# Optimization experiments

Measured on AMD Instinct MI355X. Metric: run time of the kernel, lower is better.

## Reference

```python
import jax, jax.numpy as jnp
import numpy as np

H = 512   # hidden_state_sizes
E = 512   # embedding_size
L = 2     # num_rnn_layers
VGG = 4096


def gru_cell(x, h, Wu, bu, Wr, br, Wc, bc):
    # stacked = cat(x, h) along features; rows of W: first input, then hidden
    s = jnp.concatenate([x, h], axis=1)
    r = jax.nn.sigmoid(s @ Wr + br)
    u = jax.nn.sigmoid(s @ Wu + bu)
    s1 = jnp.concatenate([x, r * h], axis=1)
    c = jnp.tanh(s1 @ Wc + bc)
    return u * h + (1.0 - u) * c


def setup_inputs() -> dict:
    key = jax.random.key(0)
    ks = jax.random.split(key, 10)
    B, T, V = 128, 40, 10000
    N = E + H  # concat width (layer0: E+H == H+H since E==H)
    sc = float(np.sqrt(1.0 / N))
    return dict(
        xTokens=jax.random.randint(ks[0], (B, T), 0, V),
        vgg_fc7=jax.random.normal(ks[1], (B, VGG), jnp.float32),
        embedding=jax.random.normal(ks[2], (V, E), jnp.float32) * 0.02,
        W_in=jax.random.normal(ks[3], (VGG, H), jnp.float32) * float(np.sqrt(1.0 / VGG)),
        b_in=jnp.zeros((H,), jnp.float32),
        W_u=jax.random.normal(ks[4], (L, N, H), jnp.float32) * sc,
        b_u=jnp.zeros((L, H), jnp.float32),
        W_r=jax.random.normal(ks[5], (L, N, H), jnp.float32) * sc,
        b_r=jnp.zeros((L, H), jnp.float32),
        W_c=jax.random.normal(ks[6], (L, N, H), jnp.float32) * sc,
        b_c=jnp.zeros((L, H), jnp.float32),
        W_out=jax.random.normal(ks[7], (H, V), jnp.float32) * float(np.sqrt(1.0 / H)),
        b_out=jnp.zeros((V,), jnp.float32),
    )


def reference(xTokens, vgg_fc7, embedding, W_in, b_in, W_u, b_u, W_r, b_r,
              W_c, b_c, W_out, b_out):
    # initial hidden state from image features, shared across rnn layers
    h0 = jnp.tanh(vgg_fc7 @ W_in + b_in)                # [B,H]
    h = jnp.broadcast_to(h0, (L,) + h0.shape)           # [L,B,H]
    x = embedding[xTokens]                              # [B,T,E]
    xs = jnp.swapaxes(x, 0, 1)                          # [T,B,E] (scan over time)

    def step(h, xt):
        hs = []
        inp = xt
        for j in range(L):  # small fixed layer loop
            hj = gru_cell(inp, h[j], W_u[j], b_u[j], W_r[j], b_r[j], W_c[j], b_c[j])
            hs.append(hj)
            inp = hj
        logit = inp @ W_out + b_out                     # [B,V]
        return jnp.stack(hs), logit

    h_final, logits = jax.lax.scan(step, h, xs)         # logits [T,B,V]
    return jnp.swapaxes(logits, 0, 1), h_final
```

## Files before the change

kernel.cpp:

```cpp
#include <hip/hip_runtime.h>
#include <hip/hip_bf16.h>
#include <math.h>

typedef __bf16 bf16_t;
typedef __bf16 bf16x8 __attribute__((ext_vector_type(8)));
typedef float  f32x4 __attribute__((ext_vector_type(4)));
typedef float  f4    __attribute__((ext_vector_type(4)));
typedef float  f2    __attribute__((ext_vector_type(2)));
typedef unsigned short u16x4 __attribute__((ext_vector_type(4)));
typedef unsigned long long u64;

#define HS  512
#define BB  128
#define TT  40
#define VV  10000
#define VGGN 4096
#define SLOT ((size_t)65536)
#define NBLK 96
#define NGRID 256

#define CL(h, idx) ((((h) * 164) + (idx)) * 64)
#define CRH0(h,s) CL(h, (s))
#define CHB0(h,s) CL(h, 41 + (s))
#define CRH1(h,s) CL(h, 82 + (s))
#define CHB1(h,s) CL(h, 123 + (s))
#define NSYNCW (328 * 64)

__device__ __forceinline__ void cst64(void* p, u64 v) {
  __hip_atomic_store((u64*)p, v, __ATOMIC_RELAXED, __HIP_MEMORY_SCOPE_AGENT);
}

__device__ __forceinline__ void slot_inc(unsigned* sync, int line)
{
  __syncthreads();
  asm volatile("" ::: "memory");
  if (threadIdx.x == 0)
    __hip_atomic_fetch_add(&sync[line], 1u, __ATOMIC_RELAXED,
                           __HIP_MEMORY_SCOPE_AGENT);
}

template<int SLP>
__device__ __forceinline__ void slot_wait(unsigned* sync, int line,
                                          unsigned target)
{
  if (threadIdx.x == 0) {
    while (__hip_atomic_load(&sync[line], __ATOMIC_RELAXED,
                             __HIP_MEMORY_SCOPE_AGENT) < target)
      __builtin_amdgcn_s_sleep(SLP);
  }
  asm volatile("" ::: "memory");
  __syncthreads();
}

template<int SLP>
__device__ __forceinline__ void slot_wait2(unsigned* sync, int lineA,
                                           unsigned tA, int lineB, unsigned tB)
{
  if (threadIdx.x == 0) {
    while (__hip_atomic_load(&sync[lineA], __ATOMIC_RELAXED,
                             __HIP_MEMORY_SCOPE_AGENT) < tA)
      __builtin_amdgcn_s_sleep(SLP);
    while (__hip_atomic_load(&sync[lineB], __ATOMIC_RELAXED,
                             __HIP_MEMORY_SCOPE_AGENT) < tB)
      __builtin_amdgcn_s_sleep(SLP);
  }
  asm volatile("" ::: "memory");
  __syncthreads();
}

__global__ void zero_sync(unsigned* p)
{
  for (int i = threadIdx.x; i < NSYNCW; i += 256) p[i] = 0u;
}

__global__ __launch_bounds__(256) void gemm_bt(
    const bf16_t* __restrict__ A, const bf16_t* __restrict__ Bt,
    const float* __restrict__ bias, float* __restrict__ C,
    int Nvalid, int ldc, int permute_tb)
{
  const int bm = blockIdx.x * 128, bn = blockIdx.y * 128;
  const int tid = threadIdx.x;
  const int wave = tid >> 6, lane = tid & 63;
  const int wm = (wave >> 1) * 64, wn = (wave & 1) * 64;
  const int l15 = lane & 15, kg = lane >> 4;
  const bf16_t* Ap = A + (size_t)(bm + wm + l15) * 512 + kg * 8;
  const bf16_t* Bp = Bt + (size_t)(bn + wn + l15) * 512 + kg * 8;
  f32x4 acc[4][4];
#pragma unroll
  for (int i = 0; i < 4; ++i)
#pragma unroll
    for (int j = 0; j < 4; ++j)
#pragma unroll
      for (int e = 0; e < 4; ++e) acc[i][j][e] = 0.f;

  for (int kk = 0; kk < 512; kk += 32) {
    bf16x8 a[4], b[4];
#pragma unroll
    for (int i = 0; i < 4; ++i) a[i] = *(const bf16x8*)(Ap + (size_t)i * 16 * 512 + kk);
#pragma unroll
    for (int j = 0; j < 4; ++j) b[j] = *(const bf16x8*)(Bp + (size_t)j * 16 * 512 + kk);
#pragma unroll
    for (int i = 0; i < 4; ++i)
#pragma unroll
      for (int j = 0; j < 4; ++j)
        acc[i][j] = __builtin_amdgcn_mfma_f32_16x16x32_bf16(a[i], b[j], acc[i][j], 0, 0, 0);
  }

#pragma unroll
  for (int fm = 0; fm < 4; ++fm) {
#pragma unroll
    for (int fn = 0; fn < 4; ++fn) {
      int n = bn + wn + fn * 16 + l15;
      if (n >= Nvalid) continue;
      float bv = bias ? bias[n] : 0.f;
#pragma unroll
      for (int e = 0; e < 4; ++e) {
        int m = bm + wm + fm * 16 + kg * 4 + e;
        int orow = permute_tb ? ((m & 127) * TT + (m >> 7)) : m;
        C[(size_t)orow * ldc + n] = acc[fm][fn][e] + bv;
      }
    }
  }
}

struct PArgs {
  const bf16_t *Btru0, *Bt1ru, *Btc0, *Btc1;
  const float  *xg0, *bu, *br, *bc, *hs0init;
  bf16_t *hb0_seq, *hb1_seq, *rh0s, *rh1s;
  const bf16_t *Wto;
  const float  *bo;
  float *out, *out_hfin;
  unsigned *sync;
};

template<int K, int NF>
__device__ __forceinline__ void tile_gemm64(
    const bf16_t* __restrict__ A0, const bf16_t* __restrict__ A1,
    const bf16_t* Bs, int wave, int lane, f32x4 (&acc)[NF])
{
  const int l15 = lane & 15, kg = lane >> 4;
  const int mw = wave * 16;
#pragma unroll
  for (int f = 0; f < NF; ++f)
#pragma unroll
    for (int e = 0; e < 4; ++e) acc[f][e] = 0.f;

#pragma unroll
  for (int kk = 0; kk < K; kk += 32) {
    const bf16_t* Asrc = (kk < 512) ? A0 : A1;
    const int kc = (kk < 512 ? kk : kk - 512) + kg * 8;
    bf16x8 a = *(const bf16x8*)(Asrc + (size_t)(mw + l15) * 512 + kc);
    bf16x8 b[NF];
#pragma unroll
    for (int f = 0; f < NF; ++f) {
      int row = f * 16 + l15;
      int byteoff = row * (2 * K) + ((2 * kk + 16 * kg) ^ ((row & 7) << 4));
      b[f] = *(const bf16x8*)((const char*)Bs + byteoff);
    }
#pragma unroll
    for (int f = 0; f < NF; ++f)
      acc[f] = __builtin_amdgcn_mfma_f32_16x16x32_bf16(a, b[f], acc[f], 0, 0, 0);
  }
}

template<int C>
__device__ __forceinline__ void publish64(
    bf16_t* dst, int row0, int n0, float (&v)[2][4],
    unsigned short (*tb)[36], int wave, int lane, int tid)
{
  const int l15 = lane & 15, kg = lane >> 4;
  const int mw = wave * 16;
  constexpr int NFp = C / 16;
#pragma unroll
  for (int f = 0; f < NFp; ++f)
#pragma unroll
    for (int e = 0; e < 4; ++e)
      tb[mw + kg * 4 + e][f * 16 + l15] =
          __builtin_bit_cast(unsigned short, (bf16_t)v[f][e]);
  __syncthreads();
  constexpr int NU = 64 * C / 4;
  constexpr int IT = (NU + 255) / 256;
#pragma unroll
  for (int it = 0; it < IT; ++it) {
    int lin = it * 256 + tid;
    if (lin < NU) {
      int row = lin / (C / 4);
      int cc  = (lin % (C / 4)) * 4;
      u16x4 pk = { tb[row][cc], tb[row][cc + 1], tb[row][cc + 2], tb[row][cc + 3] };
      cst64(dst + (size_t)(row0 + row) * 512 + n0 + cc, __builtin_bit_cast(u64, pk));
    }
  }
}

__global__ __launch_bounds__(256) void gru_persist(PArgs P)
{
  const int bid = blockIdx.x, tid = threadIdx.x;
  const int wave = tid >> 6, lane = tid & 63;
  const int l15 = lane & 15, kg = lane >> 4;
  unsigned* sync = P.sync;

  __threadfence();
  __syncthreads();

  if (bid >= NBLK) {
    const int w = bid - NBLK;
    const int wm = (wave >> 1) * 64, wn = (wave & 1) * 64;
    for (int tau = w; tau < TT * 79; tau += (NGRID - NBLK)) {
      const int t = tau / 79, nb = tau % 79;
      slot_wait2<64>(sync, CHB1(0, t + 1), 32u, CHB1(1, t + 1), 32u);
      const bf16_t* A = P.hb1_seq + (size_t)(t + 1) * SLOT;
      const bf16_t* Bp = P.Wto + (size_t)(nb * 128 + wn + l15) * 512 + kg * 8;
      f32x4 acc[4][4];
#pragma unroll
      for (int i = 0; i < 4; ++i)
#pragma unroll
        for (int j = 0; j < 4; ++j)
#pragma unroll
          for (int e = 0; e < 4; ++e) acc[i][j][e] = 0.f;
      for (int kk = 0; kk < 512; kk += 32) {
        bf16x8 a[4], b[4];
#pragma unroll
        for (int i = 0; i < 4; ++i)
          a[i] = *(const bf16x8*)(A + (size_t)(wm + i * 16 + l15) * 512 + kk + kg * 8);
#pragma unroll
        for (int j = 0; j < 4; ++j)
          b[j] = *(const bf16x8*)(Bp + (size_t)j * 16 * 512 + kk);
#pragma unroll
        for (int i = 0; i < 4; ++i)
#pragma unroll
          for (int j = 0; j < 4; ++j)
            acc[i][j] = __builtin_amdgcn_mfma_f32_16x16x32_bf16(a[i], b[j], acc[i][j], 0, 0, 0);
      }
#pragma unroll
      for (int fm = 0; fm < 4; ++fm) {
#pragma unroll
        for (int fn = 0; fn < 4; ++fn) {
          int n = nb * 128 + wn + fn * 16 + l15;
          if (n >= VV) continue;
          float bv = P.bo[n];
#pragma unroll
          for (int e = 0; e < 4; ++e) {
            int b_row = wm + fm * 16 + kg * 4 + e;
            P.out[(size_t)(b_row * TT + t) * VV + n] = acc[fm][fn][e] + bv;
          }
        }
      }
      __syncthreads();
    }
    return;
  }

  const int half = bid / 48;
  const int b2   = bid % 48;
  const int row0 = half * 64;
  const bool L0 = (b2 < 16);
  const int q  = L0 ? b2 : b2 - 16;
  const int n0 = L0 ? q * 32 : q * 16;
  const int mw = wave * 16;

  __shared__ bf16_t Bs[49152];
  __shared__ unsigned short tb[64][36];
  bf16_t* BsRU = Bs;
  bf16_t* BsC  = Bs + 32768;

  if (L0) {
    for (int c = tid; c < 4096; c += 256) {
      int row = c >> 6, cb = (c & 63) * 16;
      const bf16_t* src = (row < 32) ? P.Btru0 + (size_t)(n0 + row) * 512
                                     : P.Btru0 + (size_t)(512 + n0 + row - 32) * 512;
      *(f4*)((char*)BsRU + row * 1024 + (cb ^ ((row & 7) << 4))) =
          *(const f4*)((const char*)src + cb);
    }
    for (int c = tid; c < 2048; c += 256) {
      int row = c >> 6, cb = (c & 63) * 16;
      const bf16_t* src = P.Btc0 + (size_t)(n0 + row) * 512;
      *(f4*)((char*)BsC + row * 1024 + (cb ^ ((row & 7) << 4))) =
          *(const f4*)((const char*)src + cb);
    }
  } else {
    for (int c = tid; c < 4096; c += 256) {
      int row = c >> 7, cb = (c & 127) * 16;
      const bf16_t* src = (row < 16) ? P.Bt1ru + (size_t)(n0 + row) * 1024
                                     : P.Bt1ru + (size_t)(512 + n0 + row - 16) * 1024;
      *(f4*)((char*)BsRU + row * 2048 + (cb ^ ((row & 7) << 4))) =
          *(const f4*)((const char*)src + cb);
    }
    for (int c = tid; c < 2048; c += 256) {
      int row = c >> 7, cb = (c & 127) * 16;
      const bf16_t* src = P.Btc1 + (size_t)(n0 + row) * 1024;
      *(f4*)((char*)BsC + row * 2048 + (cb ^ ((row & 7) << 4))) =
          *(const f4*)((const char*)src + cb);
    }
  }
  __syncthreads();

  const int NFh = L0 ? 2 : 1;
  float hreg[2][4], ureg[2][4], rhv[2][4];
#pragma unroll
  for (int f = 0; f < 2; ++f)
#pragma unroll
    for (int e = 0; e < 4; ++e) {
      int row = row0 + mw + kg * 4 + e;
      hreg[f][e] = (f < NFh)
          ? P.hs0init[(size_t)row * 512 + n0 + f * 16 + l15] : 0.f;
      ureg[f][e] = 0.f; rhv[f][e] = 0.f;
    }

  if (L0) {
    for (int s = 0; s < 40; ++s) {
      if (s >= 1) slot_wait<8>(sync, CHB0(half, s), 16u);
      f32x4 acc4[4];
      const bf16_t* A0 = P.hb0_seq + (size_t)s * SLOT + (size_t)row0 * 512;
      tile_gemm64<512, 4>(A0, A0, BsRU, wave, lane, acc4);
      const float* xg = P.xg0 + (size_t)s * 128 * 1536;
#pragma unroll
      for (int f = 0; f < 2; ++f)
#pragma unroll
        for (int e = 0; e < 4; ++e) {
          int row = row0 + mw + kg * 4 + e;
          int col = n0 + f * 16 + l15;
          float pu = acc4[f][e]     + xg[(size_t)row * 1536 + col];
          float pr = acc4[f + 2][e] + xg[(size_t)row * 1536 + 512 + col];
          ureg[f][e] = 1.f / (1.f + expf(-pu));
          rhv[f][e]  = (1.f / (1.f + expf(-pr))) * hreg[f][e];
        }
      publish64<32>(P.rh0s + (size_t)s * SLOT, row0, n0, rhv, tb, wave, lane, tid);
      slot_inc(sync, CRH0(half, s));
      slot_wait<8>(sync, CRH0(half, s), 16u);

      f32x4 acc2[2];
      const bf16_t* Arh = P.rh0s + (size_t)s * SLOT + (size_t)row0 * 512;
      tile_gemm64<512, 2>(Arh, Arh, BsC, wave, lane, acc2);
#pragma unroll
      for (int f = 0; f < 2; ++f)
#pragma unroll
        for (int e = 0; e < 4; ++e) {
          int row = row0 + mw + kg * 4 + e;
          int col = n0 + f * 16 + l15;
          float c = tanhf(acc2[f][e] + xg[(size_t)row * 1536 + 1024 + col]);
          float u = ureg[f][e];
          hreg[f][e] = u * hreg[f][e] + (1.f - u) * c;
          rhv[f][e] = hreg[f][e];
        }
      publish64<32>(P.hb0_seq + (size_t)(s + 1) * SLOT, row0, n0, rhv, tb, wave, lane, tid);
      slot_inc(sync, CHB0(half, s + 1));
    }
  } else {
    for (int s = 1; s <= 40; ++s) {
      if (s >= 2) slot_wait2<8>(sync, CHB0(half, s), 16u, CHB1(half, s - 1), 32u);
      else        slot_wait<8>(sync, CHB0(half, 1), 16u);
      f32x4 acc2[2];
      tile_gemm64<1024, 2>(P.hb0_seq + (size_t)s * SLOT + (size_t)row0 * 512,
                           P.hb1_seq + (size_t)(s - 1) * SLOT + (size_t)row0 * 512,
                           BsRU, wave, lane, acc2);
      float bvu = P.bu[512 + n0 + l15];
      float bvr = P.br[512 + n0 + l15];
#pragma unroll
      for (int e = 0; e < 4; ++e) {
        float pu = acc2[0][e] + bvu;
        float pr = acc2[1][e] + bvr;
        ureg[0][e] = 1.f / (1.f + expf(-pu));
        rhv[0][e]  = (1.f / (1.f + expf(-pr))) * hreg[0][e];
      }
      publish64<16>(P.rh1s + (size_t)s * SLOT, row0, n0, rhv, tb, wave, lane, tid);
      slot_inc(sync, CRH1(half, s));
      slot_wait<8>(sync, CRH1(half, s), 32u);

      f32x4 acc1[1];
      tile_gemm64<1024, 1>(P.hb0_seq + (size_t)s * SLOT + (size_t)row0 * 512,
                           P.rh1s + (size_t)s * SLOT + (size_t)row0 * 512,
                           BsC, wave, lane, acc1);
      float bvc = P.bc[512 + n0 + l15];
#pragma unroll
      for (int e = 0; e < 4; ++e) {
        float c = tanhf(acc1[0][e] + bvc);
        float u = ureg[0][e];
        hreg[0][e] = u * hreg[0][e] + (1.f - u) * c;
        rhv[0][e] = hreg[0][e];
      }
      publish64<16>(P.hb1_seq + (size_t)s * SLOT, row0, n0, rhv, tb, wave, lane, tid);
      slot_inc(sync, CHB1(half, s));
    }
  }

  float* dst = P.out_hfin + (L0 ? 0 : 65536);
#pragma unroll
  for (int f = 0; f < 2; ++f)
    if (f < NFh)
#pragma unroll
      for (int e = 0; e < 4; ++e) {
        int row = row0 + mw + kg * 4 + e;
        dst[(size_t)row * 512 + n0 + f * 16 + l15] = hreg[f][e];
      }
}

__global__ __launch_bounds__(256) void h0_gemm(
    const bf16_t* __restrict__ vggb, const bf16_t* __restrict__ Wint,
    float* __restrict__ part)
{
  const int bn = blockIdx.x * 128, z = blockIdx.y, k0 = z * 512;
  const int tid = threadIdx.x;
  const int wave = tid >> 6, lane = tid & 63;
  const int wm = (wave >> 1) * 64, wn = (wave & 1) * 64;
  const int l15 = lane & 15, kg = lane >> 4;
  const bf16_t* Ap = vggb + (size_t)(wm + l15) * 4096 + k0 + kg * 8;
  const bf16_t* Bp = Wint + (size_t)(bn + wn + l15) * 4096 + k0 + kg * 8;
  f32x4 acc[4][4];
#pragma unroll
  for (int i = 0; i < 4; ++i)
#pragma unroll
    for (int j = 0; j < 4; ++j)
#pragma unroll
      for (int e = 0; e < 4; ++e) acc[i][j][e] = 0.f;
  for (int kk = 0; kk < 512; kk += 32) {
    bf16x8 a[4], b[4];
#pragma unroll
    for (int i = 0; i < 4; ++i) a[i] = *(const bf16x8*)(Ap + (size_t)i * 16 * 4096 + kk);
#pragma unroll
    for (int j = 0; j < 4; ++j) b[j] = *(const bf16x8*)(Bp + (size_t)j * 16 * 4096 + kk);
#pragma unroll
    for (int i = 0; i < 4; ++i)
#pragma unroll
      for (int j = 0; j < 4; ++j)
        acc[i][j] = __builtin_amdgcn_mfma_f32_16x16x32_bf16(a[i], b[j], acc[i][j], 0, 0, 0);
  }
#pragma unroll
  for (int fm = 0; fm < 4; ++fm)
#pragma unroll
    for (int fn = 0; fn < 4; ++fn) {
      int n = bn + wn + fn * 16 + l15;
#pragma unroll
      for (int e = 0; e < 4; ++e) {
        int m = wm + fm * 16 + kg * 4 + e;
        part[(size_t)z * SLOT + m * 512 + n] = acc[fm][fn][e];
      }
    }
}

__global__ void h0_fin(const float* __restrict__ part, const float* __restrict__ bin,
                       float* __restrict__ hs0init,
                       bf16_t* __restrict__ hb00, bf16_t* __restrict__ hb10)
{
  int i = blockIdx.x * 256 + threadIdx.x;
  int n = i & 511;
  float s = bin[n];
#pragma unroll
  for (int z = 0; z < 8; ++z) s += part[(size_t)z * SLOT + i];
  float v = tanhf(s);
  hs0init[i] = v;
  hb00[i] = (bf16_t)v; hb10[i] = (bf16_t)v;
}

__global__ void conv_bf16(const float* __restrict__ src, bf16_t* __restrict__ dst)
{
  int i = blockIdx.x * 256 + threadIdx.x;
  f4 v = ((const f4*)src)[i];
  dst[i * 4 + 0] = (bf16_t)v[0]; dst[i * 4 + 1] = (bf16_t)v[1];
  dst[i * 4 + 2] = (bf16_t)v[2]; dst[i * 4 + 3] = (bf16_t)v[3];
}

__global__ void gather_emb(const int* __restrict__ tok, const float* __restrict__ emb,
                           bf16_t* __restrict__ A)
{
  int m = blockIdx.x;
  int t = m >> 7, b = m & 127;
  int tk = tok[b * TT + t];
  const float* src = emb + (size_t)tk * 512;
  int i = threadIdx.x;
  f4 v = *(const f4*)(src + i * 4);
  bf16_t* dst = A + (size_t)m * 512 + i * 4;
  dst[0] = (bf16_t)v[0]; dst[1] = (bf16_t)v[1];
  dst[2] = (bf16_t)v[2]; dst[3] = (bf16_t)v[3];
}

struct TJob { const float* src; bf16_t* dst; int K; int dstld; };
struct TJobs10 { TJob j[10]; };
__global__ void transpose_gen(TJobs10 jobs)
{
  TJob jb = jobs.j[blockIdx.z];
  int k0 = blockIdx.x * 32;
  if (k0 >= jb.K) return;
  int n0 = blockIdx.y * 32;
  __shared__ float tile[32][33];
  int tx = threadIdx.x, ty = threadIdx.y;
#pragma unroll
  for (int r = 0; r < 4; ++r)
    tile[ty + 8 * r][tx] = jb.src[(size_t)(k0 + ty + 8 * r) * 512 + n0 + tx];
  __syncthreads();
#pragma unroll
  for (int r = 0; r < 4; ++r)
    jb.dst[(size_t)(n0 + ty + 8 * r) * jb.dstld + k0 + tx] = (bf16_t)tile[tx][ty + 8 * r];
}

__global__ void transpose_wout(const float* __restrict__ W, bf16_t* __restrict__ dst)
{
  __shared__ float tile[32][33];
  int k0 = blockIdx.x * 32, n0 = blockIdx.y * 32;
  int tx = threadIdx.x, ty = threadIdx.y;
#pragma unroll
  for (int r = 0; r < 4; ++r) {
    int n = n0 + tx;
    tile[ty + 8 * r][tx] = (n < VV) ? W[(size_t)(k0 + ty + 8 * r) * VV + n] : 0.f;
  }
  __syncthreads();
#pragma unroll
  for (int r = 0; r < 4; ++r)
    dst[(size_t)(n0 + ty + 8 * r) * 512 + k0 + tx] = (bf16_t)tile[tx][ty + 8 * r];
}

__global__ void build_xbias(const float* __restrict__ bu, const float* __restrict__ br,
                            const float* __restrict__ bc, float* __restrict__ xb)
{
  int i = blockIdx.x * 256 + threadIdx.x;
  if (i < 2 * 1536) {
    int j = i / 1536, qq = i % 1536;
    int g = qq >> 9, n = qq & 511;
    const float* src = (g == 0) ? bu : (g == 1) ? br : bc;
    xb[i] = src[j * 512 + n];
  }
}

extern "C" void kernel_launch(void* const* d_in, const int* in_sizes, int n_in,
                              void* d_out, int out_size, void* d_ws, size_t ws_size,
                              hipStream_t stream)
{
  const int*   tok = (const int*)  d_in[0];
  const float* vgg = (const float*)d_in[1];
  const float* emb = (const float*)d_in[2];
  const float* Win = (const float*)d_in[3];
  const float* bin = (const float*)d_in[4];
  const float* Wu  = (const float*)d_in[5];
  const float* bu  = (const float*)d_in[6];
  const float* Wr  = (const float*)d_in[7];
  const float* br  = (const float*)d_in[8];
  const float* Wc  = (const float*)d_in[9];
  const float* bc  = (const float*)d_in[10];
  const float* Wo  = (const float*)d_in[11];
  const float* bo  = (const float*)d_in[12];
  float* out = (float*)d_out;

  size_t off = 0;
  auto alloc = [&](size_t bytes) -> void* {
    void* p = (char*)d_ws + off;
    off += (bytes + 255) & ~(size_t)255;
    return p;
  };
  float*  hs0init = (float*) alloc(SLOT * 4);
  bf16_t* rh0s  = (bf16_t*)alloc(41 * SLOT * 2);
  bf16_t* rh1s  = (bf16_t*)alloc(41 * SLOT * 2);
  bf16_t* hb0_seq = (bf16_t*)alloc(41 * SLOT * 2);
  bf16_t* hb1_seq = (bf16_t*)alloc(41 * SLOT * 2);
  bf16_t* Aemb  = (bf16_t*)alloc((size_t)TT * BB * 512 * 2);
  float*  xg0   = (float*) alloc((size_t)TT * BB * 1536 * 4);
  bf16_t* Btx0  = (bf16_t*)alloc((size_t)1536 * 512 * 2);
  bf16_t* Btru0 = (bf16_t*)alloc((size_t)1024 * 512 * 2);
  bf16_t* Btc0  = (bf16_t*)alloc((size_t)512 * 512 * 2);
  bf16_t* Bt1ru = (bf16_t*)alloc((size_t)1024 * 1024 * 2);
  bf16_t* Btc1  = (bf16_t*)alloc((size_t)512 * 1024 * 2);
  bf16_t* Wto   = (bf16_t*)alloc((size_t)10112 * 512 * 2);
  bf16_t* Wint  = (bf16_t*)alloc((size_t)512 * 4096 * 2);
  bf16_t* vggb  = (bf16_t*)alloc((size_t)128 * 4096 * 2);
  float*  h0part= (float*) alloc(8 * SLOT * 4);
  float*  xbias = (float*) alloc(2 * 1536 * 4);
  unsigned* syncws = (unsigned*) alloc(NSYNCW * 4);
  if (off > ws_size) return;

  TJobs10 tj;
  tj.j[0] = { Wu,                Btx0,                512, 512 };
  tj.j[1] = { Wr,                Btx0 + 262144,       512, 512 };
  tj.j[2] = { Wc,                Btx0 + 524288,       512, 512 };
  tj.j[3] = { Wu + 262144,       Btru0,               512, 512 };
  tj.j[4] = { Wr + 262144,       Btru0 + 262144,      512, 512 };
  tj.j[5] = { Wc + 262144,       Btc0,                512, 512 };
  tj.j[6] = { Wu + 524288,       Bt1ru,               1024, 1024 };
  tj.j[7] = { Wr + 524288,       Bt1ru + 524288,      1024, 1024 };
  tj.j[8] = { Wc + 524288,       Btc1,                1024, 1024 };
  tj.j[9] = { Win,               Wint,                4096, 4096 };
  transpose_gen<<<dim3(128, 16, 10), dim3(32, 8), 0, stream>>>(tj);
  transpose_wout<<<dim3(16, 316), dim3(32, 8), 0, stream>>>(Wo, Wto);
  build_xbias<<<12, 256, 0, stream>>>(bu, br, bc, xbias);
  gather_emb<<<TT * BB, 128, 0, stream>>>(tok, emb, Aemb);
  conv_bf16<<<512, 256, 0, stream>>>(vgg, vggb);
  zero_sync<<<1, 256, 0, stream>>>(syncws);

  h0_gemm<<<dim3(4, 8), 256, 0, stream>>>(vggb, Wint, h0part);
  h0_fin<<<256, 256, 0, stream>>>(h0part, bin, hs0init, hb0_seq, hb1_seq);

  gemm_bt<<<dim3(40, 12), 256, 0, stream>>>(Aemb, Btx0, xbias, xg0, 1536, 1536, 0);

  PArgs pa;
  pa.Btru0 = Btru0; pa.Bt1ru = Bt1ru; pa.Btc0 = Btc0; pa.Btc1 = Btc1;
  pa.xg0 = xg0; pa.bu = bu; pa.br = br; pa.bc = bc; pa.hs0init = hs0init;
  pa.hb0_seq = hb0_seq; pa.hb1_seq = hb1_seq;
  pa.rh0s = rh0s; pa.rh1s = rh1s;
  pa.Wto = Wto; pa.bo = bo; pa.out = out;
  pa.out_hfin = out + (size_t)BB * TT * VV;
  pa.sync = syncws;
  gru_persist<<<NGRID, 256, 0, stream>>>(pa);
}
```

Before: 626.8 us.

## Split recurrence into quarter-batch groups with split-K layer1 and dynamic output-tile queue

The persistent GRU kernel now uses 192 recurrence blocks in four 32-row batch groups instead of 96 blocks in two 64-row halves, halving per-block work on the serial critical path. Layer-1 blocks split their K=1024 GEMMs across wave pairs and reduce partials through shared memory. Output-projection tiles are now claimed from a global atomic work queue, and recurrence blocks join that queue once their steps finish. The costs are more sync counters and more blocks to wait on per step, an extra shared-memory reduction with barriers, and fewer dedicated projection blocks while the recurrence is still running.

```diff
diff --git a/kernel.cpp b/kernel.cpp
--- a/kernel.cpp
+++ b/kernel.cpp
@@ -16,15 +16,17 @@
 #define VV  10000
 #define VGGN 4096
 #define SLOT ((size_t)65536)
-#define NBLK 96
+#define NBLK 192
 #define NGRID 256
-
-#define CL(h, idx) ((((h) * 164) + (idx)) * 64)
-#define CRH0(h,s) CL(h, (s))
-#define CHB0(h,s) CL(h, 41 + (s))
-#define CRH1(h,s) CL(h, 82 + (s))
-#define CHB1(h,s) CL(h, 123 + (s))
-#define NSYNCW (328 * 64)
+#define NTILE (TT * 79)
+
+#define CL(qt, idx) ((((qt) * 164) + (idx)) * 64)
+#define CRH0(qt,s) CL(qt, (s))
+#define CHB0(qt,s) CL(qt, 41 + (s))
+#define CRH1(qt,s) CL(qt, 82 + (s))
+#define CHB1(qt,s) CL(qt, 123 + (s))
+#define QLINE (656 * 64)
+#define NSYNCW (657 * 64)
 
 __device__ __forceinline__ void cst64(void* p, u64 v) {
   __hip_atomic_store((u64*)p, v, __ATOMIC_RELAXED, __HIP_MEMORY_SCOPE_AGENT);
@@ -133,265 +135,300 @@
   unsigned *sync;
 };
 
-template<int K, int NF>
-__device__ __forceinline__ void tile_gemm64(
-    const bf16_t* __restrict__ A0, const bf16_t* __restrict__ A1,
-    const bf16_t* Bs, int wave, int lane, f32x4 (&acc)[NF])
-{
-  const int l15 = lane & 15, kg = lane >> 4;
-  const int mw = wave * 16;
-#pragma unroll
-  for (int f = 0; f < NF; ++f)
-#pragma unroll
-    for (int e = 0; e < 4; ++e) acc[f][e] = 0.f;
-
-#pragma unroll
-  for (int kk = 0; kk < K; kk += 32) {
-    const bf16_t* Asrc = (kk < 512) ? A0 : A1;
-    const int kc = (kk < 512 ? kk : kk - 512) + kg * 8;
-    bf16x8 a = *(const bf16x8*)(Asrc + (size_t)(mw + l15) * 512 + kc);
-    bf16x8 b[NF];
-#pragma unroll
-    for (int f = 0; f < NF; ++f) {
-      int row = f * 16 + l15;
-      int byteoff = row * (2 * K) + ((2 * kk + 16 * kg) ^ ((row & 7) << 4));
-      b[f] = *(const bf16x8*)((const char*)Bs + byteoff);
-    }
-#pragma unroll
-    for (int f = 0; f < NF; ++f)
-      acc[f] = __builtin_amdgcn_mfma_f32_16x16x32_bf16(a, b[f], acc[f], 0, 0, 0);
-  }
-}
-
-template<int C>
-__device__ __forceinline__ void publish64(
-    bf16_t* dst, int row0, int n0, float (&v)[2][4],
-    unsigned short (*tb)[36], int wave, int lane, int tid)
-{
-  const int l15 = lane & 15, kg = lane >> 4;
-  const int mw = wave * 16;
-  constexpr int NFp = C / 16;
-#pragma unroll
-  for (int f = 0; f < NFp; ++f)
-#pragma unroll
-    for (int e = 0; e < 4; ++e)
-      tb[mw + kg * 4 + e][f * 16 + l15] =
-          __builtin_bit_cast(unsigned short, (bf16_t)v[f][e]);
-  __syncthreads();
-  constexpr int NU = 64 * C / 4;
-  constexpr int IT = (NU + 255) / 256;
-#pragma unroll
-  for (int it = 0; it < IT; ++it) {
-    int lin = it * 256 + tid;
-    if (lin < NU) {
-      int row = lin / (C / 4);
-      int cc  = (lin % (C / 4)) * 4;
-      u16x4 pk = { tb[row][cc], tb[row][cc + 1], tb[row][cc + 2], tb[row][cc + 3] };
-      cst64(dst + (size_t)(row0 + row) * 512 + n0 + cc, __builtin_bit_cast(u64, pk));
-    }
-  }
-}
-
 __global__ __launch_bounds__(256) void gru_persist(PArgs P)
 {
   const int bid = blockIdx.x, tid = threadIdx.x;
   const int wave = tid >> 6, lane = tid & 63;
   const int l15 = lane & 15, kg = lane >> 4;
+  const int rg = wave >> 1, wsub = wave & 1;
+  const int mwr = rg * 16;
   unsigned* sync = P.sync;
+
+  __shared__ bf16_t Bs[49152];
+  __shared__ float paccs[2][32][33];
+  __shared__ unsigned short tb[32][36];
+  __shared__ int qtile;
+  bf16_t* BsRU = Bs;
+  bf16_t* BsC  = Bs + 32768;
 
   __threadfence();
   __syncthreads();
 
-  if (bid >= NBLK) {
-    const int w = bid - NBLK;
-    const int wm = (wave >> 1) * 64, wn = (wave & 1) * 64;
-    for (int tau = w; tau < TT * 79; tau += (NGRID - NBLK)) {
-      const int t = tau / 79, nb = tau % 79;
-      slot_wait2<64>(sync, CHB1(0, t + 1), 32u, CHB1(1, t + 1), 32u);
-      const bf16_t* A = P.hb1_seq + (size_t)(t + 1) * SLOT;
-      const bf16_t* Bp = P.Wto + (size_t)(nb * 128 + wn + l15) * 512 + kg * 8;
-      f32x4 acc[4][4];
+  if (bid < NBLK) {
+    const int qt   = bid / 48;
+    const int b2   = bid % 48;
+    const int row0 = qt * 32;
+    const bool L0  = (b2 < 16);
+    const int q    = L0 ? b2 : b2 - 16;
+    const int n0   = L0 ? q * 32 : q * 16;
+
+    if (L0) {
+      for (int c = tid; c < 4096; c += 256) {
+        int row = c >> 6, cb = (c & 63) * 16;
+        const bf16_t* src = (row < 32) ? P.Btru0 + (size_t)(n0 + row) * 512
+                                       : P.Btru0 + (size_t)(512 + n0 + row - 32) * 512;
+        *(f4*)((char*)BsRU + row * 1024 + (cb ^ ((row & 7) << 4))) =
+            *(const f4*)((const char*)src + cb);
+      }
+      for (int c = tid; c < 2048; c += 256) {
+        int row = c >> 6, cb = (c & 63) * 16;
+        const bf16_t* src = P.Btc0 + (size_t)(n0 + row) * 512;
+        *(f4*)((char*)BsC + row * 1024 + (cb ^ ((row & 7) << 4))) =
+            *(const f4*)((const char*)src + cb);
+      }
+    } else {
+      for (int c = tid; c < 4096; c += 256) {
+        int row = c >> 7, cb = (c & 127) * 16;
+        const bf16_t* src = (row < 16) ? P.Bt1ru + (size_t)(n0 + row) * 1024
+                                       : P.Bt1ru + (size_t)(512 + n0 + row - 16) * 1024;
+        *(f4*)((char*)BsRU + row * 2048 + (cb ^ ((row & 7) << 4))) =
+            *(const f4*)((const char*)src + cb);
+      }
+      for (int c = tid; c < 2048; c += 256) {
+        int row = c >> 7, cb = (c & 127) * 16;
+        const bf16_t* src = P.Btc1 + (size_t)(n0 + row) * 1024;
+        *(f4*)((char*)BsC + row * 2048 + (cb ^ ((row & 7) << 4))) =
+            *(const f4*)((const char*)src + cb);
+      }
+    }
+    __syncthreads();
+
+    float hreg[4], ureg[4];
+#pragma unroll
+    for (int e = 0; e < 4; ++e) {
+      int row = row0 + mwr + kg * 4 + e;
+      int col = L0 ? (n0 + wsub * 16 + l15) : (n0 + l15);
+      hreg[e] = P.hs0init[(size_t)row * 512 + col];
+      ureg[e] = 0.f;
+    }
+
+    if (L0) {
+      for (int s = 0; s < 40; ++s) {
+        if (s >= 1) slot_wait<8>(sync, CHB0(qt, s), 16u);
+        f32x4 au, ar;
+#pragma unroll
+        for (int e = 0; e < 4; ++e) { au[e] = 0.f; ar[e] = 0.f; }
+        const bf16_t* A0 = P.hb0_seq + (size_t)s * SLOT + (size_t)row0 * 512;
+        for (int kk = 0; kk < 512; kk += 32) {
+          bf16x8 a = *(const bf16x8*)(A0 + (size_t)(mwr + l15) * 512 + kk + kg * 8);
+          int rowu = wsub * 16 + l15;
+          int rowr = 32 + wsub * 16 + l15;
+          bf16x8 bu_ = *(const bf16x8*)((const char*)BsRU + rowu * 1024 +
+                         ((2 * kk + 16 * kg) ^ ((rowu & 7) << 4)));
+          bf16x8 br_ = *(const bf16x8*)((const char*)BsRU + rowr * 1024 +
+                         ((2 * kk + 16 * kg) ^ ((rowr & 7) << 4)));
+          au = __builtin_amdgcn_mfma_f32_16x16x32_bf16(a, bu_, au, 0, 0, 0);
+          ar = __builtin_amdgcn_mfma_f32_16x16x32_bf16(a, br_, ar, 0, 0, 0);
+        }
+        const float* xg = P.xg0 + (size_t)s * 128 * 1536;
+#pragma unroll
+        for (int e = 0; e < 4; ++e) {
+          int row = row0 + mwr + kg * 4 + e;
+          int col = n0 + wsub * 16 + l15;
+          float pu = au[e] + xg[(size_t)row * 1536 + col];
+          float pr = ar[e] + xg[(size_t)row * 1536 + 512 + col];
+          ureg[e] = 1.f / (1.f + expf(-pu));
+          float rv = (1.f / (1.f + expf(-pr))) * hreg[e];
+          tb[mwr + kg * 4 + e][wsub * 16 + l15] =
+              __builtin_bit_cast(unsigned short, (bf16_t)rv);
+        }
+        __syncthreads();
+        {
+          int row = tid >> 3, cc = (tid & 7) * 4;
+          u16x4 pk = { tb[row][cc], tb[row][cc+1], tb[row][cc+2], tb[row][cc+3] };
+          cst64(P.rh0s + (size_t)s * SLOT + (size_t)(row0 + row) * 512 + n0 + cc,
+                __builtin_bit_cast(u64, pk));
+        }
+        slot_inc(sync, CRH0(qt, s));
+        slot_wait<8>(sync, CRH0(qt, s), 16u);
+        f32x4 ac;
+#pragma unroll
+        for (int e = 0; e < 4; ++e) ac[e] = 0.f;
+        const bf16_t* Ar = P.rh0s + (size_t)s * SLOT + (size_t)row0 * 512;
+        for (int kk = 0; kk < 512; kk += 32) {
+          bf16x8 a = *(const bf16x8*)(Ar + (size_t)(mwr + l15) * 512 + kk + kg * 8);
+          int rowc = wsub * 16 + l15;
+          bf16x8 bc_ = *(const bf16x8*)((const char*)BsC + rowc * 1024 +
+                         ((2 * kk + 16 * kg) ^ ((rowc & 7) << 4)));
+          ac = __builtin_amdgcn_mfma_f32_16x16x32_bf16(a, bc_, ac, 0, 0, 0);
+        }
+#pragma unroll
+        for (int e = 0; e < 4; ++e) {
+          int row = row0 + mwr + kg * 4 + e;
+          int col = n0 + wsub * 16 + l15;
+          float c = tanhf(ac[e] + xg[(size_t)row * 1536 + 1024 + col]);
+          hreg[e] = ureg[e] * hreg[e] + (1.f - ureg[e]) * c;
+          tb[mwr + kg * 4 + e][wsub * 16 + l15] =
+              __builtin_bit_cast(unsigned short, (bf16_t)hreg[e]);
+        }
+        __syncthreads();
+        {
+          int row = tid >> 3, cc = (tid & 7) * 4;
+          u16x4 pk = { tb[row][cc], tb[row][cc+1], tb[row][cc+2], tb[row][cc+3] };
+          cst64(P.hb0_seq + (size_t)(s + 1) * SLOT + (size_t)(row0 + row) * 512 + n0 + cc,
+                __builtin_bit_cast(u64, pk));
+        }
+        slot_inc(sync, CHB0(qt, s + 1));
+      }
+#pragma unroll
+      for (int e = 0; e < 4; ++e) {
+        int row = row0 + mwr + kg * 4 + e;
+        P.out_hfin[(size_t)row * 512 + n0 + wsub * 16 + l15] = hreg[e];
+      }
+    } else {
+      for (int s = 1; s <= 40; ++s) {
+        if (s >= 2) slot_wait2<8>(sync, CHB0(qt, s), 16u, CHB1(qt, s - 1), 32u);
+        else        slot_wait<8>(sync, CHB0(qt, 1), 16u);
+        f32x4 au, ar;
+#pragma unroll
+        for (int e = 0; e < 4; ++e) { au[e] = 0.f; ar[e] = 0.f; }
+        const bf16_t* Ap = (wsub ? P.hb1_seq + (size_t)(s - 1) * SLOT
+                                 : P.hb0_seq + (size_t)s * SLOT) + (size_t)row0 * 512;
+        for (int kk = 0; kk < 512; kk += 32) {
+          bf16x8 a = *(const bf16x8*)(Ap + (size_t)(mwr + l15) * 512 + kk + kg * 8);
+          int kglob = wsub * 512 + kk;
+          int rowu = l15, rowr = 16 + l15;
+          bf16x8 bu_ = *(const bf16x8*)((const char*)BsRU + rowu * 2048 +
+                         ((2 * kglob + 16 * kg) ^ ((rowu & 7) << 4)));
+          bf16x8 br_ = *(const bf16x8*)((const char*)BsRU + rowr * 2048 +
+                         ((2 * kglob + 16 * kg) ^ ((rowr & 7) << 4)));
+          au = __builtin_amdgcn_mfma_f32_16x16x32_bf16(a, bu_, au, 0, 0, 0);
+          ar = __builtin_amdgcn_mfma_f32_16x16x32_bf16(a, br_, ar, 0, 0, 0);
+        }
+#pragma unroll
+        for (int e = 0; e < 4; ++e) {
+          paccs[wsub][mwr + kg * 4 + e][l15]      = au[e];
+          paccs[wsub][mwr + kg * 4 + e][16 + l15] = ar[e];
+        }
+        __syncthreads();
+        if (wsub == 0) {
+          float bvu = P.bu[512 + n0 + l15];
+          float bvr = P.br[512 + n0 + l15];
+#pragma unroll
+          for (int e = 0; e < 4; ++e) {
+            int r = mwr + kg * 4 + e;
+            float su = paccs[0][r][l15] + paccs[1][r][l15] + bvu;
+            float sr = paccs[0][r][16 + l15] + paccs[1][r][16 + l15] + bvr;
+            ureg[e] = 1.f / (1.f + expf(-su));
+            float rv = (1.f / (1.f + expf(-sr))) * hreg[e];
+            tb[r][l15] = __builtin_bit_cast(unsigned short, (bf16_t)rv);
+          }
+        }
+        __syncthreads();
+        if (tid < 128) {
+          int row = tid >> 2, cc = (tid & 3) * 4;
+          u16x4 pk = { tb[row][cc], tb[row][cc+1], tb[row][cc+2], tb[row][cc+3] };
+          cst64(P.rh1s + (size_t)s * SLOT + (size_t)(row0 + row) * 512 + n0 + cc,
+                __builtin_bit_cast(u64, pk));
+        }
+        slot_inc(sync, CRH1(qt, s));
+        slot_wait<8>(sync, CRH1(qt, s), 32u);
+        f32x4 ac;
+#pragma unroll
+        for (int e = 0; e < 4; ++e) ac[e] = 0.f;
+        const bf16_t* Ac = (wsub ? P.rh1s + (size_t)s * SLOT
+                                 : P.hb0_seq + (size_t)s * SLOT) + (size_t)row0 * 512;
+        for (int kk = 0; kk < 512; kk += 32) {
+          bf16x8 a = *(const bf16x8*)(Ac + (size_t)(mwr + l15) * 512 + kk + kg * 8);
+          int kglob = wsub * 512 + kk;
+          int rowc = l15;
+          bf16x8 bc_ = *(const bf16x8*)((const char*)BsC + rowc * 2048 +
+                         ((2 * kglob + 16 * kg) ^ ((rowc & 7) << 4)));
+          ac = __builtin_amdgcn_mfma_f32_16x16x32_bf16(a, bc_, ac, 0, 0, 0);
+        }
+#pragma unroll
+        for (int e = 0; e < 4; ++e)
+          paccs[wsub][mwr + kg * 4 + e][l15] = ac[e];
+        __syncthreads();
+        if (wsub == 0) {
+          float bvc = P.bc[512 + n0 + l15];
+#pragma unroll
+          for (int e = 0; e < 4; ++e) {
+            int r = mwr + kg * 4 + e;
+            float c = tanhf(paccs[0][r][l15] + paccs[1][r][l15] + bvc);
+            hreg[e] = ureg[e] * hreg[e] + (1.f - ureg[e]) * c;
+            tb[r][l15] = __builtin_bit_cast(unsigned short, (bf16_t)hreg[e]);
+          }
+        }
+        __syncthreads();
+        if (tid < 128) {
+          int row = tid >> 2, cc = (tid & 3) * 4;
+          u16x4 pk = { tb[row][cc], tb[row][cc+1], tb[row][cc+2], tb[row][cc+3] };
+          cst64(P.hb1_seq + (size_t)s * SLOT + (size_t)(row0 + row) * 512 + n0 + cc,
+                __builtin_bit_cast(u64, pk));
+        }
+        slot_inc(sync, CHB1(qt, s));
+      }
+      if (wsub == 0) {
+#pragma unroll
+        for (int e = 0; e < 4; ++e) {
+          int row = row0 + mwr + kg * 4 + e;
+          P.out_hfin[65536 + (size_t)row * 512 + n0 + l15] = hreg[e];
+        }
+      }
+      __syncthreads();
+    }
+  }
+
+  const int wm = (wave >> 1) * 64, wn = (wave & 1) * 64;
+  for (;;) {
+    if (tid == 0)
+      qtile = (int)__hip_atomic_fetch_add(&sync[QLINE], 1u,
+                                          __ATOMIC_RELAXED, __HIP_MEMORY_SCOPE_AGENT);
+    __syncthreads();
+    int tau = qtile;
+    __syncthreads();
+    if (tau >= NTILE) break;
+    const int t = tau / 79, nb = tau % 79;
+    if (tid == 0) {
+#pragma unroll
+      for (int qq = 0; qq < 4; ++qq) {
+        while (__hip_atomic_load(&sync[CHB1(qq, t + 1)], __ATOMIC_RELAXED,
+                                 __HIP_MEMORY_SCOPE_AGENT) < 32u)
+          __builtin_amdgcn_s_sleep(16);
+      }
+    }
+    asm volatile("" ::: "memory");
+    __syncthreads();
+    const bf16_t* A = P.hb1_seq + (size_t)(t + 1) * SLOT;
+    const bf16_t* Bp = P.Wto + (size_t)(nb * 128 + wn + l15) * 512 + kg * 8;
+    f32x4 acc[4][4];
+#pragma unroll
+    for (int i = 0; i < 4; ++i)
+#pragma unroll
+      for (int j = 0; j < 4; ++j)
+#pragma unroll
+        for (int e = 0; e < 4; ++e) acc[i][j][e] = 0.f;
+    for (int kk = 0; kk < 512; kk += 32) {
+      bf16x8 a[4], b[4];
 #pragma unroll
       for (int i = 0; i < 4; ++i)
+        a[i] = *(const bf16x8*)(A + (size_t)(wm + i * 16 + l15) * 512 + kk + kg * 8);
+#pragma unroll
+      for (int j = 0; j < 4; ++j)
+        b[j] = *(const bf16x8*)(Bp + (size_t)j * 16 * 512 + kk);
+#pragma unroll
+      for (int i = 0; i < 4; ++i)
 #pragma unroll
         for (int j = 0; j < 4; ++j)
-#pragma unroll
-          for (int e = 0; e < 4; ++e) acc[i][j][e] = 0.f;
-      for (int kk = 0; kk < 512; kk += 32) {
-        bf16x8 a[4], b[4];
-#pragma unroll
-        for (int i = 0; i < 4; ++i)
-          a[i] = *(const bf16x8*)(A + (size_t)(wm + i * 16 + l15) * 512 + kk + kg * 8);
-#pragma unroll
-        for (int j = 0; j < 4; ++j)
-          b[j] = *(const bf16x8*)(Bp + (size_t)j * 16 * 512 + kk);
-#pragma unroll
-        for (int i = 0; i < 4; ++i)
-#pragma unroll
-          for (int j = 0; j < 4; ++j)
-            acc[i][j] = __builtin_amdgcn_mfma_f32_16x16x32_bf16(a[i], b[j], acc[i][j], 0, 0, 0);
-      }
-#pragma unroll
-      for (int fm = 0; fm < 4; ++fm) {
-#pragma unroll
-        for (int fn = 0; fn < 4; ++fn) {
-          int n = nb * 128 + wn + fn * 16 + l15;
-          if (n >= VV) continue;
-          float bv = P.bo[n];
-#pragma unroll
-          for (int e = 0; e < 4; ++e) {
-            int b_row = wm + fm * 16 + kg * 4 + e;
-            P.out[(size_t)(b_row * TT + t) * VV + n] = acc[fm][fn][e] + bv;
-          }
-        }
-      }
-      __syncthreads();
-    }
-    return;
-  }
-
-  const int half = bid / 48;
-  const int b2   = bid % 48;
-  const int row0 = half * 64;
-  const bool L0 = (b2 < 16);
-  const int q  = L0 ? b2 : b2 - 16;
-  const int n0 = L0 ? q * 32 : q * 16;
-  const int mw = wave * 16;
-
-  __shared__ bf16_t Bs[49152];
-  __shared__ unsigned short tb[64][36];
-  bf16_t* BsRU = Bs;
-  bf16_t* BsC  = Bs + 32768;
-
-  if (L0) {
-    for (int c = tid; c < 4096; c += 256) {
-      int row = c >> 6, cb = (c & 63) * 16;
-      const bf16_t* src = (row < 32) ? P.Btru0 + (size_t)(n0 + row) * 512
-                                     : P.Btru0 + (size_t)(512 + n0 + row - 32) * 512;
-      *(f4*)((char*)BsRU + row * 1024 + (cb ^ ((row & 7) << 4))) =
-          *(const f4*)((const char*)src + cb);
-    }
-    for (int c = tid; c < 2048; c += 256) {
-      int row = c >> 6, cb = (c & 63) * 16;
-      const bf16_t* src = P.Btc0 + (size_t)(n0 + row) * 512;
-      *(f4*)((char*)BsC + row * 1024 + (cb ^ ((row & 7) << 4))) =
-          *(const f4*)((const char*)src + cb);
-    }
-  } else {
-    for (int c = tid; c < 4096; c += 256) {
-      int row = c >> 7, cb = (c & 127) * 16;
-      const bf16_t* src = (row < 16) ? P.Bt1ru + (size_t)(n0 + row) * 1024
-                                     : P.Bt1ru + (size_t)(512 + n0 + row - 16) * 1024;
-      *(f4*)((char*)BsRU + row * 2048 + (cb ^ ((row & 7) << 4))) =
-          *(const f4*)((const char*)src + cb);
-    }
-    for (int c = tid; c < 2048; c += 256) {
-      int row = c >> 7, cb = (c & 127) * 16;
-      const bf16_t* src = P.Btc1 + (size_t)(n0 + row) * 1024;
-      *(f4*)((char*)BsC + row * 2048 + (cb ^ ((row & 7) << 4))) =
-          *(const f4*)((const char*)src + cb);
-    }
-  }
-  __syncthreads();
-
-  const int NFh = L0 ? 2 : 1;
-  float hreg[2][4], ureg[2][4], rhv[2][4];
-#pragma unroll
-  for (int f = 0; f < 2; ++f)
-#pragma unroll
-    for (int e = 0; e < 4; ++e) {
-      int row = row0 + mw + kg * 4 + e;
-      hreg[f][e] = (f < NFh)
-          ? P.hs0init[(size_t)row * 512 + n0 + f * 16 + l15] : 0.f;
-      ureg[f][e] = 0.f; rhv[f][e] = 0.f;
-    }
-
-  if (L0) {
-    for (int s = 0; s < 40; ++s) {
-      if (s >= 1) slot_wait<8>(sync, CHB0(half, s), 16u);
-      f32x4 acc4[4];
-      const bf16_t* A0 = P.hb0_seq + (size_t)s * SLOT + (size_t)row0 * 512;
-      tile_gemm64<512, 4>(A0, A0, BsRU, wave, lane, acc4);
-      const float* xg = P.xg0 + (size_t)s * 128 * 1536;
-#pragma unroll
-      for (int f = 0; f < 2; ++f)
+          acc[i][j] = __builtin_amdgcn_mfma_f32_16x16x32_bf16(a[i], b[j], acc[i][j], 0, 0, 0);
+    }
+#pragma unroll
+    for (int fm = 0; fm < 4; ++fm) {
+#pragma unroll
+      for (int fn = 0; fn < 4; ++fn) {
+        int n = nb * 128 + wn + fn * 16 + l15;
+        if (n >= VV) continue;
+        float bv = P.bo[n];
 #pragma unroll
         for (int e = 0; e < 4; ++e) {
-          int row = row0 + mw + kg * 4 + e;
-          int col = n0 + f * 16 + l15;
-          float pu = acc4[f][e]     + xg[(size_t)row * 1536 + col];
-          float pr = acc4[f + 2][e] + xg[(size_t)row * 1536 + 512 + col];
-          ureg[f][e] = 1.f / (1.f + expf(-pu));
-          rhv[f][e]  = (1.f / (1.f + expf(-pr))) * hreg[f][e];
-        }
-      publish64<32>(P.rh0s + (size_t)s * SLOT, row0, n0, rhv, tb, wave, lane, tid);
-      slot_inc(sync, CRH0(half, s));
-      slot_wait<8>(sync, CRH0(half, s), 16u);
-
-      f32x4 acc2[2];
-      const bf16_t* Arh = P.rh0s + (size_t)s * SLOT + (size_t)row0 * 512;
-      tile_gemm64<512, 2>(Arh, Arh, BsC, wave, lane, acc2);
-#pragma unroll
-      for (int f = 0; f < 2; ++f)
-#pragma unroll
-        for (int e = 0; e < 4; ++e) {
-          int row = row0 + mw + kg * 4 + e;
-          int col = n0 + f * 16 + l15;
-          float c = tanhf(acc2[f][e] + xg[(size_t)row * 1536 + 1024 + col]);
-          float u = ureg[f][e];
-          hreg[f][e] = u * hreg[f][e] + (1.f - u) * c;
-          rhv[f][e] = hreg[f][e];
-        }
-      publish64<32>(P.hb0_seq + (size_t)(s + 1) * SLOT, row0, n0, rhv, tb, wave, lane, tid);
-      slot_inc(sync, CHB0(half, s + 1));
-    }
-  } else {
-    for (int s = 1; s <= 40; ++s) {
-      if (s >= 2) slot_wait2<8>(sync, CHB0(half, s), 16u, CHB1(half, s - 1), 32u);
-      else        slot_wait<8>(sync, CHB0(half, 1), 16u);
-      f32x4 acc2[2];
-      tile_gemm64<1024, 2>(P.hb0_seq + (size_t)s * SLOT + (size_t)row0 * 512,
-                           P.hb1_seq + (size_t)(s - 1) * SLOT + (size_t)row0 * 512,
-                           BsRU, wave, lane, acc2);
-      float bvu = P.bu[512 + n0 + l15];
-      float bvr = P.br[512 + n0 + l15];
-#pragma unroll
-      for (int e = 0; e < 4; ++e) {
-        float pu = acc2[0][e] + bvu;
-        float pr = acc2[1][e] + bvr;
-        ureg[0][e] = 1.f / (1.f + expf(-pu));
-        rhv[0][e]  = (1.f / (1.f + expf(-pr))) * hreg[0][e];
-      }
-      publish64<16>(P.rh1s + (size_t)s * SLOT, row0, n0, rhv, tb, wave, lane, tid);
-      slot_inc(sync, CRH1(half, s));
-      slot_wait<8>(sync, CRH1(half, s), 32u);
-
-      f32x4 acc1[1];
-      tile_gemm64<1024, 1>(P.hb0_seq + (size_t)s * SLOT + (size_t)row0 * 512,
-                           P.rh1s + (size_t)s * SLOT + (size_t)row0 * 512,
-                           BsC, wave, lane, acc1);
-      float bvc = P.bc[512 + n0 + l15];
-#pragma unroll
-      for (int e = 0; e < 4; ++e) {
-        float c = tanhf(acc1[0][e] + bvc);
-        float u = ureg[0][e];
-        hreg[0][e] = u * hreg[0][e] + (1.f - u) * c;
-        rhv[0][e] = hreg[0][e];
-      }
-      publish64<16>(P.hb1_seq + (size_t)s * SLOT, row0, n0, rhv, tb, wave, lane, tid);
-      slot_inc(sync, CHB1(half, s));
-    }
-  }
-
-  float* dst = P.out_hfin + (L0 ? 0 : 65536);
-#pragma unroll
-  for (int f = 0; f < 2; ++f)
-    if (f < NFh)
-#pragma unroll
-      for (int e = 0; e < 4; ++e) {
-        int row = row0 + mw + kg * 4 + e;
-        dst[(size_t)row * 512 + n0 + f * 16 + l15] = hreg[f][e];
-      }
+          int b_row = wm + fm * 16 + kg * 4 + e;
+          P.out[(size_t)(b_row * TT + t) * VV + n] = acc[fm][fn][e] + bv;
+        }
+      }
+    }
+    __syncthreads();
+  }
 }
 
 __global__ __launch_bounds__(256) void h0_gemm(
```

After: 658.6 us. +5.1%, slower.
